# Optimization experiments

Hardware: AMD Instinct MI355X
Metric: run time of the kernel (lower is better)

The kernel has to match this reference:

```python
import jax, jax.numpy as jnp
import numpy as np

N = 768          # n_nuclei
EMB = 32         # embedding_dim
RBF = 32         # rbf_dim
CUTOFF = 10.0    # rbf_cutoff
MAXQ = 10        # max(charges)


def _edges(n):
    # fully-connected edge list exactly as in GNN.__call__
    senders = np.arange(n).repeat(n - 1)
    recv = np.arange(n)[None].repeat(n - 1, axis=0)
    recv = (recv + np.arange(n - 1)[:, None] + 1) % n
    return jnp.asarray(senders), jnp.asarray(recv.reshape(-1))


def _mlp2(x, w0, b0, w1, b1=None):
    # AutoMLP(out_dim, depth=2): Dense+silu, Dense (final_bias optional)
    h = jax.nn.silu(x @ w0 + b0)
    y = h @ w1
    return y if b1 is None else y + b1


def _seg_mean(vals, seg, n):
    s = jax.ops.segment_sum(vals, seg, num_segments=n, indices_are_sorted=True)
    c = jax.ops.segment_sum(jnp.ones((vals.shape[0], 1), vals.dtype), seg,
                            num_segments=n, indices_are_sorted=True)
    return s / jnp.maximum(c, 1.0)


def setup_inputs() -> dict:
    key = jax.random.key(0)
    ki = iter(jax.random.split(key, 48))

    def W(din, dout):
        return jax.random.normal(next(ki), (din, dout), jnp.float32) / np.sqrt(din).astype(np.float32)

    def b(d):
        return jax.random.normal(next(ki), (d,), jnp.float32) * 0.01

    return dict(
        nuclei=jax.random.normal(next(ki), (N, 3), jnp.float32) * 3.0,
        charges=jax.random.randint(next(ki), (N,), 0, MAXQ),
        f=(jnp.arange(RBF, dtype=jnp.float32) + 1.0) * jnp.pi,  # BesselRBF param init
        embed_table=jax.random.normal(next(ki), (MAXQ, EMB), jnp.float32),
        mp1_w0=W(96, 32), mp1_b0=b(32), mp1_w1=W(32, 32), mp1_b1=b(32),
        up1_w0=W(64, 64), up1_b0=b(64), up1_w1=W(64, 64), up1_b1=b(64),
        mp2_w0=W(160, 32), mp2_b0=b(32), mp2_w1=W(32, 32), mp2_b1=b(32),
        up2_w0=W(96, 64), up2_b0=b(64), up2_w1=W(64, 64), up2_b1=b(64),
        no_w0=W(160, 3), no_b0=b(3), no_w1=W(3, 3),
        no_embed=jax.random.normal(next(ki), (MAXQ, 3), jnp.float32) * 0.1,
        go_w0=W(160, 1), go_b0=b(1), go_w1=W(1, 1), go_b1=b(1),
    )


def reference(nuclei, charges, f, embed_table,
              mp1_w0, mp1_b0, mp1_w1, mp1_b1,
              up1_w0, up1_b0, up1_w1, up1_b1,
              mp2_w0, mp2_b0, mp2_w1, mp2_b1,
              up2_w0, up2_b0, up2_w1, up2_b1,
              no_w0, no_b0, no_w1, no_embed,
              go_w0, go_b0, go_w1, go_b1):
    nuclei = nuclei.reshape(-1, 3) @ jnp.eye(3, dtype=nuclei.dtype)  # constants 'axes'
    n = nuclei.shape[0]
    senders, receivers = _edges(n)

    # BesselRBF on pairwise distances
    d = jnp.linalg.norm(nuclei[senders] - nuclei[receivers], axis=-1)
    x_ext = d[:, None] + 1e-8
    e_embed = jnp.sqrt(2.0 / CUTOFF) * jnp.sin(f * x_ext / CUTOFF) / x_ext  # [E, RBF]

    n_embed = embed_table[charges]  # [N, EMB]
    embeddings = [n_embed]

    # layer 1: msg out 32, update out 64 (no residual: 32 != 64)
    edge_in = jnp.concatenate([n_embed[senders], n_embed[receivers], e_embed], axis=-1)
    msg = _seg_mean(_mlp2(edge_in, mp1_w0, mp1_b0, mp1_w1, mp1_b1), senders, n)
    upd = _mlp2(jnp.concatenate([n_embed, msg], axis=-1), up1_w0, up1_b0, up1_w1, up1_b1)
    n_embed = upd  # dims differ -> plain replacement
    embeddings.append(n_embed)

    # layer 2: msg out 32, update out 64 (residual: 64 == 64)
    edge_in = jnp.concatenate([n_embed[senders], n_embed[receivers], e_embed], axis=-1)
    msg = _seg_mean(_mlp2(edge_in, mp2_w0, mp2_b0, mp2_w1, mp2_b1), senders, n)
    upd = _mlp2(jnp.concatenate([n_embed, msg], axis=-1), up2_w0, up2_b0, up2_w1, up2_b1)
    n_embed = n_embed + upd
    embeddings.append(n_embed)

    agg = jnp.concatenate(embeddings, axis=-1)  # [N, 32+64+64=160]

    node_out = _mlp2(agg, no_w0, no_b0, no_w1) + no_embed[charges]  # [N, 3]
    global_out = _mlp2(jnp.mean(agg, axis=0), go_w0, go_b0, go_w1, go_b1)  # [1]
    return (node_out, global_out)
```

## Files before the change

kernel.cpp:

```cpp
#include <hip/hip_runtime.h>
#include <hip/hip_bf16.h>

typedef __hip_bfloat16 bf16;
typedef __attribute__((ext_vector_type(8))) short short8;
typedef __attribute__((ext_vector_type(4))) float float4v;

#define NN   768
#define NEPS 767

#define C_NUC   0
#define C_F     2304
#define C_MP1W0 2656
#define C_MP1B0 5728
#define C_MP1W1 5760
#define C_MP1B1 6784
#define C_UP1W0 6816
#define C_UP1B0 10912
#define C_UP1W1 10976
#define C_UP1B1 15072
#define C_MP2W0 15136
#define C_MP2B0 20256
#define C_MP2W1 20288
#define C_MP2B1 21312
#define C_UP2W0 21344
#define C_UP2B0 27488
#define C_UP2W1 27552
#define C_UP2B1 31648
#define C_NOW0  31712
#define C_NOB0  32192
#define C_NOW1  32195
#define C_NOEMB 32204
#define C_GOW0  32234
#define C_GOB0  32394
#define C_GOW1  32395
#define C_GOB1  32396
__device__ __align__(16) float g_c[32400];

#define OFF_EMB0 0
#define OFF_SA1  24576
#define OFF_SB1  49152
#define OFF_EMB1 73728
#define OFF_SA2  122880
#define OFF_SB2  147456
__device__ float g_ws[172032];
__device__ float g_agg[640];
__device__ int   g_cnt;
__device__ int   g_isf;

struct Ptrs { const void* p[28]; };

__device__ __forceinline__ float b2f(bf16 v){ return __bfloat162float(v); }
__device__ __forceinline__ float LD(const void* p, int i, int f32){
  return f32 ? ((const float*)p)[i] : b2f(((const bf16*)p)[i]);
}
__device__ __forceinline__ int detect_f32(const void* f){
  float v = ((const float*)f)[0];
  return (fabsf(v - 3.14159265f) < 0.01f) ? 1 : 0;
}
__device__ __forceinline__ float fast_rcp(float x){ return __builtin_amdgcn_rcpf(x); }
__device__ __forceinline__ float silu_f(float p){ return p * fast_rcp(1.f + __expf(-p)); }
__device__ __forceinline__ unsigned short rne_bf16(float x){
  unsigned int b = __float_as_uint(x);
  return (unsigned short)((b + 0x7fffu + ((b >> 16) & 1u)) >> 16);
}
__device__ __forceinline__ void cv(const void* p, int off, int sz, int gt, int isf){
  for (int i = gt; i < sz; i += 96*256) g_c[off + i] = LD(p, i, isf);
}

__launch_bounds__(256)
__global__ void k_conv_prep(Ptrs P, const int* __restrict__ charges){
  int t = threadIdx.x;
  int gt = blockIdx.x*256 + t;
  int isf = detect_f32(P.p[2]);
  if (gt == 0){ g_isf = isf; g_cnt = 0; }
  if (gt < 640) g_agg[gt] = 0.f;

  cv(P.p[0],  C_NUC,   2304, gt, isf);
  cv(P.p[2],  C_F,     32,   gt, isf);
  cv(P.p[4],  C_MP1W0, 3072, gt, isf);
  cv(P.p[5],  C_MP1B0, 32,   gt, isf);
  cv(P.p[6],  C_MP1W1, 1024, gt, isf);
  cv(P.p[7],  C_MP1B1, 32,   gt, isf);
  cv(P.p[8],  C_UP1W0, 4096, gt, isf);
  cv(P.p[9],  C_UP1B0, 64,   gt, isf);
  cv(P.p[10], C_UP1W1, 4096, gt, isf);
  cv(P.p[11], C_UP1B1, 64,   gt, isf);
  cv(P.p[12], C_MP2W0, 5120, gt, isf);
  cv(P.p[13], C_MP2B0, 32,   gt, isf);
  cv(P.p[14], C_MP2W1, 1024, gt, isf);
  cv(P.p[15], C_MP2B1, 32,   gt, isf);
  cv(P.p[16], C_UP2W0, 6144, gt, isf);
  cv(P.p[17], C_UP2B0, 64,   gt, isf);
  cv(P.p[18], C_UP2W1, 4096, gt, isf);
  cv(P.p[19], C_UP2B1, 64,   gt, isf);
  cv(P.p[20], C_NOW0,  480,  gt, isf);
  cv(P.p[21], C_NOB0,  3,    gt, isf);
  cv(P.p[22], C_NOW1,  9,    gt, isf);
  cv(P.p[23], C_NOEMB, 30,   gt, isf);
  cv(P.p[24], C_GOW0,  160,  gt, isf);
  cv(P.p[25], C_GOB0,  1,    gt, isf);
  cv(P.p[26], C_GOW1,  1,    gt, isf);
  cv(P.p[27], C_GOB1,  1,    gt, isf);

  __shared__ float w0L[2048];
  __shared__ float rowL[8][32];
  for (int idx = t; idx < 2048; idx += 256) w0L[idx] = LD(P.p[4], idx, isf);
  int nd = t >> 5, col = t & 31;
  int node = blockIdx.x*8 + nd;
  int ch = charges[node];
  float v = LD(P.p[3], ch*32 + col, isf);
  g_ws[OFF_EMB0 + node*32 + col] = v;
  rowL[nd][col] = v;
  __syncthreads();
  float sa = 0.f, sb = 0.f;
  #pragma unroll
  for (int k = 0; k < 32; k++){
    float rv = rowL[nd][k];
    sa = fmaf(rv, w0L[k*32 + col],      sa);
    sb = fmaf(rv, w0L[(32+k)*32 + col], sb);
  }
  g_ws[OFF_SA1 + node*32 + col] = sa;
  g_ws[OFF_SB1 + node*32 + col] = sb;
}

#define EDGE_LOOP(SA_OFF, SB_OFF, W0E, B0, W1, B1)                                   \
  {                                                                                  \
    const float* SA = g_ws + (SA_OFF);                                               \
    const float* SB = g_ws + (SB_OFF);                                               \
    {                                                                                \
      const float4* src = (const float4*)(g_c + C_NUC);                              \
      float4* dst = (float4*)pos;                                                    \
      for (int idx = t; idx < 576; idx += 256) dst[idx] = src[idx];                  \
      ((float4*)w1L)[t] = ((const float4*)(g_c + (W1)))[t];                          \
    }                                                                                \
    short8 bfr0, bfr1;                                                               \
    _Pragma("unroll")                                                                \
    for (int j = 0; j < 8; j++){                                                     \
      int row = q*8 + j;                                                             \
      bfr0[j] = (short)rne_bf16(g_c[(W0E) + row*32 + c]);                            \
      bfr1[j] = (short)rne_bf16(g_c[(W0E) + row*32 + 16 + c]);                       \
    }                                                                                \
    float preB0 = SA[i*32 + c]      + g_c[(B0) + c];                                 \
    float preB1 = SA[i*32 + 16 + c] + g_c[(B0) + 16 + c];                            \
    float fj[8];                                                                     \
    _Pragma("unroll")                                                                \
    for (int j = 0; j < 8; j++) fj[j] = g_c[C_F + q*8 + j] * 0.1f;                   \
    __syncthreads();                                                                 \
    float px = pos[i*3], py = pos[i*3+1], pz = pos[i*3+2];                           \
    float sum0 = 0.f, sum1 = 0.f;                                                    \
    for (int tl = w; tl < 48; tl += 4){                                              \
      int el = tl*16 + c;                                                            \
      int ela = (el < NEPS) ? el : 0;                                                \
      int r = ela + (ela >= i);                                                      \
      float dx = px - pos[r*3], dy = py - pos[r*3+1], dz = pz - pos[r*3+2];          \
      float d  = sqrtf(fmaf(dx, dx, fmaf(dy, dy, dz*dz)));                           \
      float xs = d + 1e-8f;                                                          \
      float scv = 0.44721359549995793f * fast_rcp(xs);                               \
      short8 af;                                                                     \
      _Pragma("unroll")                                                              \
      for (int j = 0; j < 8; j++) af[j] = (short)rne_bf16(scv * __sinf(fj[j]*xs));   \
      float4v z = {0.f, 0.f, 0.f, 0.f};                                              \
      float4v a0 = __builtin_amdgcn_mfma_f32_16x16x32_bf16(af, bfr0, z, 0, 0, 0);    \
      float4v a1 = __builtin_amdgcn_mfma_f32_16x16x32_bf16(af, bfr1, z, 0, 0, 0);    \
      _Pragma("unroll")                                                              \
      for (int p = 0; p < 4; p++){                                                   \
        int el2 = tl*16 + q*4 + p;                                                   \
        if (el2 < NEPS){                                                             \
          int r2 = el2 + (el2 >= i);                                                 \
          float v0 = a0[p] + preB0 + SB[r2*32 + c];                                  \
          float v1 = a1[p] + preB1 + SB[r2*32 + 16 + c];                             \
          sum0 += silu_f(v0);                                                        \
          sum1 += silu_f(v1);                                                        \
        }                                                                            \
      }                                                                              \
    }                                                                                \
    sum0 += __shfl_xor(sum0, 16); sum0 += __shfl_xor(sum0, 32);                      \
    sum1 += __shfl_xor(sum1, 16); sum1 += __shfl_xor(sum1, 32);                      \
    if (lane < 16){ wsum[w][lane] = sum0; wsum[w][16 + lane] = sum1; }               \
    __syncthreads();                                                                 \
    if (t < 32) hsumL[t] = wsum[0][t] + wsum[1][t] + wsum[2][t] + wsum[3][t];        \
    __syncthreads();                                                                 \
    if (t < 32){                                                                     \
      float y = 0.f;                                                                 \
      _Pragma("unroll")                                                              \
      for (int m = 0; m < 32; m++) y = fmaf(hsumL[m], w1L[m*32 + t], y);             \
      msgL[t] = y * (1.f/767.f) + g_c[(B1) + t];                                     \
    }                                                                                \
  }

__launch_bounds__(256)
__global__ void k_edge1(){
  __shared__ __align__(16) float pos[NN*3];
  __shared__ __align__(16) float w1L[1024];
  __shared__ float wsum[4][32];
  __shared__ float hsumL[32];
  __shared__ float msgL[32];
  __shared__ float catU[64];
  __shared__ float hU[64];
  __shared__ float e1U[64];
  __shared__ float part[256];

  int i = blockIdx.x, t = threadIdx.x;
  int w = t >> 6, lane = t & 63, q = lane >> 4, c = lane & 15;

  EDGE_LOOP(OFF_SA1, OFF_SB1, C_MP1W0 + 2048, C_MP1B0, C_MP1W1, C_MP1B1)

  if (t < 32){
    catU[t] = g_ws[OFF_EMB0 + i*32 + t];
    catU[32 + t] = msgL[t];
  }
  __syncthreads();

  int g = t >> 6, col = t & 63;
  {
    const float* w0 = g_c + C_UP1W0;
    float p0 = 0.f;
    #pragma unroll
    for (int j = 0; j < 16; j++){ int k = g*16 + j; p0 = fmaf(catU[k], w0[k*64 + col], p0); }
    part[t] = p0;
  }
  __syncthreads();
  if (t < 64) hU[t] = silu_f(g_c[C_UP1B0 + t] + part[t] + part[64+t] + part[128+t] + part[192+t]);
  __syncthreads();
  {
    const float* w1u = g_c + C_UP1W1;
    float p1 = 0.f;
    #pragma unroll
    for (int j = 0; j < 16; j++){ int k = g*16 + j; p1 = fmaf(hU[k], w1u[k*64 + col], p1); }
    part[t] = p1;
  }
  __syncthreads();
  if (t < 64){
    float y = g_c[C_UP1B1 + t] + part[t] + part[64+t] + part[128+t] + part[192+t];
    e1U[t] = y;
    g_ws[OFF_EMB1 + i*64 + t] = y;
  }
  __syncthreads();
  {
    int half = t >> 7, g2 = (t >> 5) & 3, c32 = t & 31;
    const float* m2 = g_c + C_MP2W0;
    float p2 = 0.f;
    #pragma unroll
    for (int j = 0; j < 16; j++){
      int k = g2*16 + j;
      p2 = fmaf(e1U[k], m2[(half*64 + k)*32 + c32], p2);
    }
    part[t] = p2;
  }
  __syncthreads();
  if (t < 64){
    int half = t >> 5, c32 = t & 31;
    float s = part[half*128 + c32] + part[half*128 + 32 + c32]
            + part[half*128 + 64 + c32] + part[half*128 + 96 + c32];
    if (half == 0) g_ws[OFF_SA2 + i*32 + c32] = s;
    else           g_ws[OFF_SB2 + i*32 + c32] = s;
  }
}

__launch_bounds__(256)
__global__ void k_edge2(const int* __restrict__ charges, void* __restrict__ out){
  __shared__ __align__(16) float pos[NN*3];
  __shared__ __align__(16) float w1L[1024];
  __shared__ float wsum[4][32];
  __shared__ float hsumL[32];
  __shared__ float msgL[32];
  __shared__ float catU[96];
  __shared__ float hU[64];
  __shared__ float aggL[160];
  __shared__ float noL[522];
  __shared__ float h3L[3];
  __shared__ float part[256];
  __shared__ int lastL;

  int i = blockIdx.x, t = threadIdx.x;
  int w = t >> 6, lane = t & 63, q = lane >> 4, c = lane & 15;

  EDGE_LOOP(OFF_SA2, OFF_SB2, C_MP2W0 + 4096, C_MP2B0, C_MP2W1, C_MP2B1)

  if (t < 64) catU[t] = g_ws[OFF_EMB1 + i*64 + t];
  if (t < 32){ catU[64 + t] = msgL[t]; aggL[t] = g_ws[OFF_EMB0 + i*32 + t]; }
  for (int idx = t; idx < 522; idx += 256) noL[idx] = g_c[C_NOW0 + idx];
  __syncthreads();

  int g = t >> 6, col = t & 63;
  {
    const float* w0 = g_c + C_UP2W0;
    float p0 = 0.f;
    #pragma unroll
    for (int j = 0; j < 24; j++){ int k = g*24 + j; p0 = fmaf(catU[k], w0[k*64 + col], p0); }
    part[t] = p0;
  }
  __syncthreads();
  if (t < 64) hU[t] = silu_f(g_c[C_UP2B0 + t] + part[t] + part[64+t] + part[128+t] + part[192+t]);
  __syncthreads();
  {
    const float* w1u = g_c + C_UP2W1;
    float p1 = 0.f;
    #pragma unroll
    for (int j = 0; j < 16; j++){ int k = g*16 + j; p1 = fmaf(hU[k], w1u[k*64 + col], p1); }
    part[t] = p1;
  }
  __syncthreads();
  if (t < 64){
    float y = g_c[C_UP2B1 + t] + part[t] + part[64+t] + part[128+t] + part[192+t];
    float e2 = catU[t] + y;
    aggL[32 + t] = catU[t];
    aggL[96 + t] = e2;
  }
  __syncthreads();
  if (t < 48){
    int chunk = t / 3, c3 = t - chunk*3;
    float p = 0.f;
    #pragma unroll
    for (int j = 0; j < 10; j++){ int k = chunk*10 + j; p = fmaf(aggL[k], noL[k*3 + c3], p); }
    part[t] = p;
  }
  __syncthreads();
  if (t < 3){
    float p = noL[480 + t];
    #pragma unroll
    for (int ch = 0; ch < 16; ch++) p += part[ch*3 + t];
    h3L[t] = silu_f(p);
  }
  __syncthreads();
  if (t < 3){
    float o = 0.f;
    #pragma unroll
    for (int m = 0; m < 3; m++) o = fmaf(h3L[m], noL[483 + m*3 + t], o);
    o += noL[492 + charges[i]*3 + t];
    if (g_isf) ((float*)out)[i*3 + t] = o;
    else       ((bf16*)out)[i*3 + t] = __float2bfloat16(o);
  }
  if (t < 160) atomicAdd(&g_agg[(i & 3)*160 + t], aggL[t]);
  __syncthreads();
  if (t == 0) lastL = (atomicAdd(&g_cnt, 1) == NN - 1) ? 1 : 0;
  __syncthreads();
  if (lastL){
    float v = 0.f;
    if (t < 160){
      float s = atomicAdd(&g_agg[t], 0.f) + atomicAdd(&g_agg[160 + t], 0.f)
              + atomicAdd(&g_agg[320 + t], 0.f) + atomicAdd(&g_agg[480 + t], 0.f);
      v = s * (1.f/768.f) * g_c[C_GOW0 + t];
    }
    part[t] = v;
    __syncthreads();
    if (t == 0){
      float tot = 0.f;
      for (int k = 0; k < 160; k++) tot += part[k];
      float h = silu_f(tot + g_c[C_GOB0]);
      float go = h * g_c[C_GOW1] + g_c[C_GOB1];
      if (g_isf) ((float*)out)[2304] = go;
      else       ((bf16*)out)[2304] = __float2bfloat16(go);
    }
  }
}

extern "C" void kernel_launch(void* const* d_in, const int* in_sizes, int n_in,
                              void* d_out, int out_size, void* d_ws, size_t ws_size,
                              hipStream_t stream) {
  Ptrs P;
  for (int k = 0; k < 28; k++) P.p[k] = d_in[k];
  const int* charges = (const int*)d_in[1];

  k_conv_prep<<<96, 256, 0, stream>>>(P, charges);
  k_edge1<<<NN, 256, 0, stream>>>();
  k_edge2<<<NN, 256, 0, stream>>>(charges, d_out);
}
```

Baseline: 178.6 us.

## Cache bf16 RBF edge features from edge layer 1 for reuse in layer 2

The first edge kernel now writes its bf16 radial-basis MFMA operand fragments to a global buffer. The second edge kernel reads them back instead of recomputing distances and sines, so it no longer needs nuclei positions in shared memory. Both kernels also issue the SB neighbour loads ahead of use: layer 1 precomputes distances per tile, and layer 2 double-buffers the next tile's loads. This trades transcendental work in layer 2 for about 37 MB of extra global writes and reads within one call.

```diff
diff --git a/kernel.cpp b/kernel.cpp
--- a/kernel.cpp
+++ b/kernel.cpp
@@ -46,6 +46,7 @@
 __device__ float g_agg[640];
 __device__ int   g_cnt;
 __device__ int   g_isf;
+__device__ short8 g_rbf[NN*48*64];
 
 struct Ptrs { const void* p[28]; };
 
@@ -123,71 +124,6 @@
   g_ws[OFF_SB1 + node*32 + col] = sb;
 }
 
-#define EDGE_LOOP(SA_OFF, SB_OFF, W0E, B0, W1, B1)                                   \
-  {                                                                                  \
-    const float* SA = g_ws + (SA_OFF);                                               \
-    const float* SB = g_ws + (SB_OFF);                                               \
-    {                                                                                \
-      const float4* src = (const float4*)(g_c + C_NUC);                              \
-      float4* dst = (float4*)pos;                                                    \
-      for (int idx = t; idx < 576; idx += 256) dst[idx] = src[idx];                  \
-      ((float4*)w1L)[t] = ((const float4*)(g_c + (W1)))[t];                          \
-    }                                                                                \
-    short8 bfr0, bfr1;                                                               \
-    _Pragma("unroll")                                                                \
-    for (int j = 0; j < 8; j++){                                                     \
-      int row = q*8 + j;                                                             \
-      bfr0[j] = (short)rne_bf16(g_c[(W0E) + row*32 + c]);                            \
-      bfr1[j] = (short)rne_bf16(g_c[(W0E) + row*32 + 16 + c]);                       \
-    }                                                                                \
-    float preB0 = SA[i*32 + c]      + g_c[(B0) + c];                                 \
-    float preB1 = SA[i*32 + 16 + c] + g_c[(B0) + 16 + c];                            \
-    float fj[8];                                                                     \
-    _Pragma("unroll")                                                                \
-    for (int j = 0; j < 8; j++) fj[j] = g_c[C_F + q*8 + j] * 0.1f;                   \
-    __syncthreads();                                                                 \
-    float px = pos[i*3], py = pos[i*3+1], pz = pos[i*3+2];                           \
-    float sum0 = 0.f, sum1 = 0.f;                                                    \
-    for (int tl = w; tl < 48; tl += 4){                                              \
-      int el = tl*16 + c;                                                            \
-      int ela = (el < NEPS) ? el : 0;                                                \
-      int r = ela + (ela >= i);                                                      \
-      float dx = px - pos[r*3], dy = py - pos[r*3+1], dz = pz - pos[r*3+2];          \
-      float d  = sqrtf(fmaf(dx, dx, fmaf(dy, dy, dz*dz)));                           \
-      float xs = d + 1e-8f;                                                          \
-      float scv = 0.44721359549995793f * fast_rcp(xs);                               \
-      short8 af;                                                                     \
-      _Pragma("unroll")                                                              \
-      for (int j = 0; j < 8; j++) af[j] = (short)rne_bf16(scv * __sinf(fj[j]*xs));   \
-      float4v z = {0.f, 0.f, 0.f, 0.f};                                              \
-      float4v a0 = __builtin_amdgcn_mfma_f32_16x16x32_bf16(af, bfr0, z, 0, 0, 0);    \
-      float4v a1 = __builtin_amdgcn_mfma_f32_16x16x32_bf16(af, bfr1, z, 0, 0, 0);    \
-      _Pragma("unroll")                                                              \
-      for (int p = 0; p < 4; p++){                                                   \
-        int el2 = tl*16 + q*4 + p;                                                   \
-        if (el2 < NEPS){                                                             \
-          int r2 = el2 + (el2 >= i);                                                 \
-          float v0 = a0[p] + preB0 + SB[r2*32 + c];                                  \
-          float v1 = a1[p] + preB1 + SB[r2*32 + 16 + c];                             \
-          sum0 += silu_f(v0);                                                        \
-          sum1 += silu_f(v1);                                                        \
-        }                                                                            \
-      }                                                                              \
-    }                                                                                \
-    sum0 += __shfl_xor(sum0, 16); sum0 += __shfl_xor(sum0, 32);                      \
-    sum1 += __shfl_xor(sum1, 16); sum1 += __shfl_xor(sum1, 32);                      \
-    if (lane < 16){ wsum[w][lane] = sum0; wsum[w][16 + lane] = sum1; }               \
-    __syncthreads();                                                                 \
-    if (t < 32) hsumL[t] = wsum[0][t] + wsum[1][t] + wsum[2][t] + wsum[3][t];        \
-    __syncthreads();                                                                 \
-    if (t < 32){                                                                     \
-      float y = 0.f;                                                                 \
-      _Pragma("unroll")                                                              \
-      for (int m = 0; m < 32; m++) y = fmaf(hsumL[m], w1L[m*32 + t], y);             \
-      msgL[t] = y * (1.f/767.f) + g_c[(B1) + t];                                     \
-    }                                                                                \
-  }
-
 __launch_bounds__(256)
 __global__ void k_edge1(){
   __shared__ __align__(16) float pos[NN*3];
@@ -195,15 +131,88 @@
   __shared__ float wsum[4][32];
   __shared__ float hsumL[32];
   __shared__ float msgL[32];
-  __shared__ float catU[64];
-  __shared__ float hU[64];
-  __shared__ float e1U[64];
-  __shared__ float part[256];
+  __shared__ float catU[64], hU[64], e1U[64], part[256];
 
   int i = blockIdx.x, t = threadIdx.x;
   int w = t >> 6, lane = t & 63, q = lane >> 4, c = lane & 15;
 
-  EDGE_LOOP(OFF_SA1, OFF_SB1, C_MP1W0 + 2048, C_MP1B0, C_MP1W1, C_MP1B1)
+  {
+    const float4* src = (const float4*)(g_c + C_NUC);
+    float4* dst = (float4*)pos;
+    for (int idx = t; idx < 576; idx += 256) dst[idx] = src[idx];
+    ((float4*)w1L)[t] = ((const float4*)(g_c + C_MP1W1))[t];
+  }
+  const float* SA = g_ws + OFF_SA1;
+  const float* SB = g_ws + OFF_SB1;
+  short8 bfr0, bfr1;
+  #pragma unroll
+  for (int j = 0; j < 8; j++){
+    int row = q*8 + j;
+    bfr0[j] = (short)rne_bf16(g_c[C_MP1W0 + 2048 + row*32 + c]);
+    bfr1[j] = (short)rne_bf16(g_c[C_MP1W0 + 2048 + row*32 + 16 + c]);
+  }
+  float preB0 = SA[i*32 + c]      + g_c[C_MP1B0 + c];
+  float preB1 = SA[i*32 + 16 + c] + g_c[C_MP1B0 + 16 + c];
+  float fj[8];
+  #pragma unroll
+  for (int j = 0; j < 8; j++) fj[j] = g_c[C_F + q*8 + j] * 0.1f;
+  __syncthreads();
+
+  float px = pos[i*3], py = pos[i*3+1], pz = pos[i*3+2];
+
+  float xs[12], scv[12];
+  #pragma unroll
+  for (int s = 0; s < 12; s++){
+    int el = (w + s*4)*16 + c;
+    int ela = (el < NEPS) ? el : 0;
+    int r = ela + (ela >= i);
+    float dx = px - pos[r*3], dy = py - pos[r*3+1], dz = pz - pos[r*3+2];
+    float d = sqrtf(fmaf(dx, dx, fmaf(dy, dy, dz*dz)));
+    xs[s] = d + 1e-8f;
+    scv[s] = 0.44721359549995793f * fast_rcp(xs[s]);
+  }
+
+  float sum0 = 0.f, sum1 = 0.f;
+  #pragma unroll 4
+  for (int s = 0; s < 12; s++){
+    int tl = w + s*4;
+    float sb0[4], sb1[4];
+    #pragma unroll
+    for (int p = 0; p < 4; p++){
+      int el2 = tl*16 + q*4 + p;
+      int e2a = (el2 < NEPS) ? el2 : 0;
+      int r2 = e2a + (e2a >= i);
+      sb0[p] = SB[r2*32 + c];
+      sb1[p] = SB[r2*32 + 16 + c];
+    }
+    short8 af;
+    #pragma unroll
+    for (int j = 0; j < 8; j++) af[j] = (short)rne_bf16(scv[s] * __sinf(fj[j]*xs[s]));
+    g_rbf[(i*48 + tl)*64 + lane] = af;
+    float4v z = {0.f, 0.f, 0.f, 0.f};
+    float4v a0 = __builtin_amdgcn_mfma_f32_16x16x32_bf16(af, bfr0, z, 0, 0, 0);
+    float4v a1 = __builtin_amdgcn_mfma_f32_16x16x32_bf16(af, bfr1, z, 0, 0, 0);
+    #pragma unroll
+    for (int p = 0; p < 4; p++){
+      int el2 = tl*16 + q*4 + p;
+      if (el2 < NEPS){
+        sum0 += silu_f(a0[p] + preB0 + sb0[p]);
+        sum1 += silu_f(a1[p] + preB1 + sb1[p]);
+      }
+    }
+  }
+  sum0 += __shfl_xor(sum0, 16); sum0 += __shfl_xor(sum0, 32);
+  sum1 += __shfl_xor(sum1, 16); sum1 += __shfl_xor(sum1, 32);
+  if (lane < 16){ wsum[w][lane] = sum0; wsum[w][16 + lane] = sum1; }
+  __syncthreads();
+  if (t < 32) hsumL[t] = wsum[0][t] + wsum[1][t] + wsum[2][t] + wsum[3][t];
+  __syncthreads();
+  if (t < 32){
+    float y = 0.f;
+    #pragma unroll
+    for (int m = 0; m < 32; m++) y = fmaf(hsumL[m], w1L[m*32 + t], y);
+    msgL[t] = y * (1.f/767.f) + g_c[C_MP1B1 + t];
+  }
 
   if (t < 32){
     catU[t] = g_ws[OFF_EMB0 + i*32 + t];
@@ -259,23 +268,86 @@
 
 __launch_bounds__(256)
 __global__ void k_edge2(const int* __restrict__ charges, void* __restrict__ out){
-  __shared__ __align__(16) float pos[NN*3];
   __shared__ __align__(16) float w1L[1024];
   __shared__ float wsum[4][32];
   __shared__ float hsumL[32];
   __shared__ float msgL[32];
-  __shared__ float catU[96];
-  __shared__ float hU[64];
-  __shared__ float aggL[160];
-  __shared__ float noL[522];
-  __shared__ float h3L[3];
-  __shared__ float part[256];
+  __shared__ float catU[96], hU[64], aggL[160], noL[522], h3L[3], part[256];
   __shared__ int lastL;
 
   int i = blockIdx.x, t = threadIdx.x;
   int w = t >> 6, lane = t & 63, q = lane >> 4, c = lane & 15;
 
-  EDGE_LOOP(OFF_SA2, OFF_SB2, C_MP2W0 + 4096, C_MP2B0, C_MP2W1, C_MP2B1)
+  ((float4*)w1L)[t] = ((const float4*)(g_c + C_MP2W1))[t];
+  const float* SA = g_ws + OFF_SA2;
+  const float* SB = g_ws + OFF_SB2;
+  short8 bfr0, bfr1;
+  #pragma unroll
+  for (int j = 0; j < 8; j++){
+    int row = q*8 + j;
+    bfr0[j] = (short)rne_bf16(g_c[C_MP2W0 + 4096 + row*32 + c]);
+    bfr1[j] = (short)rne_bf16(g_c[C_MP2W0 + 4096 + row*32 + 16 + c]);
+  }
+  float preB0 = SA[i*32 + c]      + g_c[C_MP2B0 + c];
+  float preB1 = SA[i*32 + 16 + c] + g_c[C_MP2B0 + 16 + c];
+
+  float sum0 = 0.f, sum1 = 0.f;
+  short8 afA = g_rbf[(i*48 + w)*64 + lane];
+  float sbA0[4], sbA1[4];
+  #pragma unroll
+  for (int p = 0; p < 4; p++){
+    int el2 = w*16 + q*4 + p;
+    int e2a = (el2 < NEPS) ? el2 : 0;
+    int r2 = e2a + (e2a >= i);
+    sbA0[p] = SB[r2*32 + c];
+    sbA1[p] = SB[r2*32 + 16 + c];
+  }
+  #pragma unroll
+  for (int s = 0; s < 12; s++){
+    int tl = w + s*4;
+    short8 afB;
+    float sbB0[4], sbB1[4];
+    if (s < 11){
+      int tn = tl + 4;
+      afB = g_rbf[(i*48 + tn)*64 + lane];
+      #pragma unroll
+      for (int p = 0; p < 4; p++){
+        int el2 = tn*16 + q*4 + p;
+        int e2a = (el2 < NEPS) ? el2 : 0;
+        int r2 = e2a + (e2a >= i);
+        sbB0[p] = SB[r2*32 + c];
+        sbB1[p] = SB[r2*32 + 16 + c];
+      }
+    }
+    float4v z = {0.f, 0.f, 0.f, 0.f};
+    float4v a0 = __builtin_amdgcn_mfma_f32_16x16x32_bf16(afA, bfr0, z, 0, 0, 0);
+    float4v a1 = __builtin_amdgcn_mfma_f32_16x16x32_bf16(afA, bfr1, z, 0, 0, 0);
+    #pragma unroll
+    for (int p = 0; p < 4; p++){
+      int el2 = tl*16 + q*4 + p;
+      if (el2 < NEPS){
+        sum0 += silu_f(a0[p] + preB0 + sbA0[p]);
+        sum1 += silu_f(a1[p] + preB1 + sbA1[p]);
+      }
+    }
+    if (s < 11){
+      afA = afB;
+      #pragma unroll
+      for (int p = 0; p < 4; p++){ sbA0[p] = sbB0[p]; sbA1[p] = sbB1[p]; }
+    }
+  }
+  sum0 += __shfl_xor(sum0, 16); sum0 += __shfl_xor(sum0, 32);
+  sum1 += __shfl_xor(sum1, 16); sum1 += __shfl_xor(sum1, 32);
+  if (lane < 16){ wsum[w][lane] = sum0; wsum[w][16 + lane] = sum1; }
+  __syncthreads();
+  if (t < 32) hsumL[t] = wsum[0][t] + wsum[1][t] + wsum[2][t] + wsum[3][t];
+  __syncthreads();
+  if (t < 32){
+    float y = 0.f;
+    #pragma unroll
+    for (int m = 0; m < 32; m++) y = fmaf(hsumL[m], w1L[m*32 + t], y);
+    msgL[t] = y * (1.f/767.f) + g_c[C_MP2B1 + t];
+  }
 
   if (t < 64) catU[t] = g_ws[OFF_EMB1 + i*64 + t];
   if (t < 32){ catU[64 + t] = msgL[t]; aggL[t] = g_ws[OFF_EMB0 + i*32 + t]; }
```

Measured after the change: 164.8 us. 1.08x faster.
